# Optimization experiments

Measured on AMD Instinct MI355X. Metric: run time of the kernel, lower is better.

Reference implementation:

```python
import jax, jax.numpy as jnp
import numpy as np

B, DM, NH, NL, NP = 4, 768, 12, 3, 4
HD = DM // NH
H_IMG, W_IMG = 896, 896
LEVELS = [(H_IMG // 8, W_IMG // 8), (H_IMG // 16, W_IMG // 16), (H_IMG // 32, W_IMG // 32)]
QH, QW = H_IMG // 14, W_IMG // 14
LQ = QH * QW            # 4096 query tokens (stride-14 ViT grid)
LIN = sum(h * w for h, w in LEVELS)  # 16464 multi-scale value tokens


def setup_inputs() -> dict:
    key = jax.random.key(0)
    ks = jax.random.split(key, 14)
    s = 0.02
    return {
        "query": jax.random.normal(ks[0], (B, LQ, DM), jnp.float32),
        "feat": jax.random.normal(ks[1], (B, LIN, DM), jnp.float32),
        "ln_q_g": jnp.ones((DM,), jnp.float32),
        "ln_q_b": jnp.zeros((DM,), jnp.float32),
        "ln_f_g": jnp.ones((DM,), jnp.float32),
        "ln_f_b": jnp.zeros((DM,), jnp.float32),
        "W_off": jax.random.normal(ks[2], (DM, NH * NL * NP * 2), jnp.float32) * s,
        "b_off": jax.random.normal(ks[3], (NH * NL * NP * 2,), jnp.float32) * s,
        "W_attn": jax.random.normal(ks[4], (DM, NH * NL * NP), jnp.float32) * s,
        "b_attn": jax.random.normal(ks[5], (NH * NL * NP,), jnp.float32) * s,
        "W_val": jax.random.normal(ks[6], (DM, DM), jnp.float32) * s,
        "b_val": jnp.zeros((DM,), jnp.float32),
        "W_out": jax.random.normal(ks[7], (DM, DM), jnp.float32) * s,
        "b_out": jnp.zeros((DM,), jnp.float32),
        "gamma": jax.random.normal(ks[8], (DM,), jnp.float32) * s,
    }


def _ln(x, g, b, eps=1e-6):
    m = x.mean(-1, keepdims=True)
    v = ((x - m) ** 2).mean(-1, keepdims=True)
    return (x - m) * jax.lax.rsqrt(v + eps) * g + b


def _ref_points():
    # get_reference_points for the stride-14 query grid; pixel-center coords normalized
    ry, rx = jnp.meshgrid(
        (jnp.arange(QH, dtype=jnp.float32) + 0.5) / QH,
        (jnp.arange(QW, dtype=jnp.float32) + 0.5) / QW,
        indexing="ij",
    )
    return jnp.stack([rx.reshape(-1), ry.reshape(-1)], -1)  # (LQ, 2) in (x, y)


def _sample_level(v, loc, h_, w_):
    # v: (B, h_, w_, NH, HD); loc: (B, LQ, NH, NP, 2) normalized [0,1]
    # torch grid_sample bilinear, align_corners=False, zero padding
    x = loc[..., 0] * w_ - 0.5
    y = loc[..., 1] * h_ - 0.5
    x0 = jnp.floor(x)
    y0 = jnp.floor(y)
    wx = (x - x0)[..., None]
    wy = (y - y0)[..., None]
    x0i = x0.astype(jnp.int32)
    y0i = y0.astype(jnp.int32)
    bi = jnp.arange(B)[:, None, None, None]
    hi = jnp.arange(NH)[None, None, :, None]

    def g(yi, xi):
        valid = ((xi >= 0) & (xi < w_) & (yi >= 0) & (yi < h_)).astype(v.dtype)
        got = v[bi, jnp.clip(yi, 0, h_ - 1), jnp.clip(xi, 0, w_ - 1), hi]  # (B,LQ,NH,NP,HD)
        return got * valid[..., None]

    v00 = g(y0i, x0i)
    v01 = g(y0i, x0i + 1)
    v10 = g(y0i + 1, x0i)
    v11 = g(y0i + 1, x0i + 1)
    return v00 * (1 - wx) * (1 - wy) + v01 * wx * (1 - wy) + v10 * (1 - wx) * wy + v11 * wx * wy


def _injector(query, feat, ln_q_g, ln_q_b, ln_f_g, ln_f_b, W_off, b_off, W_attn, b_attn,
              W_val, b_val, W_out, b_out, gamma):
    q = _ln(query, ln_q_g, ln_q_b)
    f = _ln(feat, ln_f_g, ln_f_b)
    value = (f @ W_val + b_val).reshape(B, LIN, NH, HD)
    off = (q @ W_off + b_off).reshape(B, LQ, NH, NL, NP, 2)
    aw = jax.nn.softmax((q @ W_attn + b_attn).reshape(B, LQ, NH, NL * NP), axis=-1)
    aw = aw.reshape(B, LQ, NH, NL, NP)
    ref = _ref_points()  # (LQ, 2)
    offset_norm = jnp.array([[w, h] for h, w in LEVELS], jnp.float32)  # (NL, 2) = (W_, H_)
    loc = ref[None, :, None, None, None, :] + off / offset_norm[None, None, None, :, None, :]
    outs = []
    start = 0
    for lvl, (h_, w_) in enumerate(LEVELS):
        v = value[:, start:start + h_ * w_].reshape(B, h_, w_, NH, HD)
        outs.append(_sample_level(v, loc[:, :, :, lvl], h_, w_))
        start += h_ * w_
    samp = jnp.stack(outs, axis=3)  # (B, LQ, NH, NL, NP, HD)
    attn_out = (samp * aw[..., None]).sum(axis=(3, 4)).reshape(B, LQ, DM)
    attn_out = attn_out @ W_out + b_out
    return query + gamma * attn_out


def reference(query, feat, ln_q_g, ln_q_b, ln_f_g, ln_f_b, W_off, b_off, W_attn, b_attn,
              W_val, b_val, W_out, b_out, gamma):
    return _injector(query, feat, ln_q_g, ln_q_b, ln_f_g, ln_f_b, W_off, b_off, W_attn,
                     b_attn, W_val, b_val, W_out, b_out, gamma)
```

## Files before the change

kernel.cpp:

```cpp
#include <hip/hip_runtime.h>
#include <hip/hip_bf16.h>

typedef __hip_bfloat16 bf16;

#define BB    4
#define LQ    4096
#define LIN   16464
#define DM    768
#define NH    12
#define HD    64
#define K_DIM 768

typedef __attribute__((ext_vector_type(8))) __bf16 bfrag;
typedef __attribute__((ext_vector_type(4))) float  ffrag;

__device__ __forceinline__ void g2l16(const void* g, void* l) {
    __builtin_amdgcn_global_load_lds(
        (const __attribute__((address_space(1))) void*)g,
        (__attribute__((address_space(3))) void*)l, 16, 0, 0);
}

__device__ __forceinline__ int xcd_swz(int orig, int nwg) {
    int xcd = orig & 7, within = orig >> 3;
    int q = nwg >> 3, r = nwg & 7;
    return (xcd < r ? xcd * (q + 1) : r * (q + 1) + (xcd - r) * q) + within;
}

__global__ __launch_bounds__(256) void ln_kernel(
    const float* __restrict__ x, const float* __restrict__ g,
    const float* __restrict__ beta, bf16* __restrict__ y)
{
    int r = blockIdx.x * 4 + (threadIdx.x >> 6);
    int lane = threadIdx.x & 63;
    const float4* xr = (const float4*)(x + (size_t)r * DM);
    float4 v[3];
    #pragma unroll
    for (int i = 0; i < 3; i++) v[i] = xr[lane + 64 * i];
    float s = 0.f, ss = 0.f;
    #pragma unroll
    for (int i = 0; i < 3; i++) {
        s  += v[i].x + v[i].y + v[i].z + v[i].w;
        ss += v[i].x * v[i].x + v[i].y * v[i].y + v[i].z * v[i].z + v[i].w * v[i].w;
    }
    #pragma unroll
    for (int m = 1; m <= 32; m <<= 1) {
        s  += __shfl_xor(s, m);
        ss += __shfl_xor(ss, m);
    }
    float mean = s * (1.f / DM);
    float inv  = rsqrtf(ss * (1.f / DM) - mean * mean + 1e-6f);
    bf16* yr = y + (size_t)r * DM;
    #pragma unroll
    for (int i = 0; i < 3; i++) {
        float4 gg = ((const float4*)g)[lane + 64 * i];
        float4 bb = ((const float4*)beta)[lane + 64 * i];
        union { bf16 h[4]; uint2 u; } p;
        p.h[0] = __float2bfloat16((v[i].x - mean) * inv * gg.x + bb.x);
        p.h[1] = __float2bfloat16((v[i].y - mean) * inv * gg.y + bb.y);
        p.h[2] = __float2bfloat16((v[i].z - mean) * inv * gg.z + bb.z);
        p.h[3] = __float2bfloat16((v[i].w - mean) * inv * gg.w + bb.w);
        *(uint2*)(yr + (lane + 64 * i) * 4) = p.u;
    }
}

__global__ __launch_bounds__(256) void cast_transpose(
    const float* __restrict__ W, bf16* __restrict__ Wt, int N)
{
    __shared__ float t[32][33];
    int n0 = blockIdx.x * 32, k0 = blockIdx.y * 32;
    int tx = threadIdx.x & 31, ty = threadIdx.x >> 5;
    #pragma unroll
    for (int i = 0; i < 4; i++) {
        int k = k0 + ty + i * 8;
        int n = n0 + tx;
        t[ty + i * 8][tx] = (n < N) ? W[(size_t)k * N + n] : 0.f;
    }
    __syncthreads();
    #pragma unroll
    for (int i = 0; i < 4; i++) {
        int n = n0 + ty + i * 8;
        Wt[(size_t)n * K_DIM + k0 + tx] = __float2bfloat16(t[tx][ty + i * 8]);
    }
}

__global__ __launch_bounds__(256) void mfma_gemm(
    const bf16*  __restrict__ A,
    const bf16*  __restrict__ Bt,
    const float* __restrict__ bias,
    void*        __restrict__ C,
    const float* __restrict__ resid,
    const float* __restrict__ gamma,
    const float* __restrict__ bias2,
    int M, int N, int mode, int nsplit)
{
    __shared__ __align__(16) char lds[32768];

    int tid  = threadIdx.x;
    int lane = tid & 63;

    int nwg  = gridDim.x * gridDim.y;
    int orig = blockIdx.y * gridDim.x + blockIdx.x;
    int wg = xcd_swz(orig, nwg);
    int bn = (wg % gridDim.x) * 128;
    int bm = (wg / gridDim.x) * 128;

    int wave = tid >> 6;
    int wr = (wave & 1) * 64, wc = (wave >> 1) * 64;

    ffrag acc[4][4] = {};

    int c0 = tid, c1 = tid + 256;
    int r0 = c0 >> 2, kb0 = (c0 & 3) * 8;
    int r1 = c1 >> 2, kb1 = (c1 & 3) * 8;
    int ra0 = min(bm + r0, M - 1), ra1 = min(bm + r1, M - 1);
    const bf16* gA0 = A  + (size_t)ra0 * K_DIM + kb0;
    const bf16* gA1 = A  + (size_t)ra1 * K_DIM + kb1;
    const bf16* gB0 = Bt + (size_t)(bn + r0) * K_DIM + kb0;
    const bf16* gB1 = Bt + (size_t)(bn + r1) * K_DIM + kb1;

    int mrow = lane & 15;
    int kq   = (lane >> 4) * 8;

    for (int k0 = 0; k0 < K_DIM; k0 += 64) {
        #pragma unroll
        for (int s = 0; s < 2; s++) {
            char* As = lds + s * 16384;
            char* Bs = As + 8192;
            int ko = k0 + s * 32;
            g2l16(gA0 + ko, As + c0 * 16);
            g2l16(gA1 + ko, As + c1 * 16);
            g2l16(gB0 + ko, Bs + c0 * 16);
            g2l16(gB1 + ko, Bs + c1 * 16);
        }
        __syncthreads();
        #pragma unroll
        for (int s = 0; s < 2; s++) {
            char* As = lds + s * 16384;
            char* Bs = As + 8192;
            bfrag a[4], b[4];
            #pragma unroll
            for (int t = 0; t < 4; t++) {
                a[t] = *(const bfrag*)(As + ((wr + t * 16 + mrow) * 32 + kq) * 2);
                b[t] = *(const bfrag*)(Bs + ((wc + t * 16 + mrow) * 32 + kq) * 2);
            }
            #pragma unroll
            for (int i = 0; i < 4; i++)
                #pragma unroll
                for (int j = 0; j < 4; j++)
                    acc[i][j] = __builtin_amdgcn_mfma_f32_16x16x32_bf16(
                        a[i], b[j], acc[i][j], 0, 0, 0);
        }
        __syncthreads();
    }

    int q4 = (lane >> 4) * 4;
    #pragma unroll
    for (int i = 0; i < 4; i++) {
        #pragma unroll
        for (int rr = 0; rr < 4; rr++) {
            int rg = bm + wr + i * 16 + q4 + rr;
            if (rg < M) {
                #pragma unroll
                for (int j = 0; j < 4; j++) {
                    int cg = bn + wc + j * 16 + mrow;
                    if (cg < N) {
                        float bv = (mode == 3 && cg >= nsplit) ? bias2[cg - nsplit]
                                                               : bias[cg];
                        float v = acc[i][j][rr] + bv;
                        size_t idx = (size_t)rg * N + cg;
                        if (mode == 0)      ((bf16*)C)[idx]  = __float2bfloat16(v);
                        else if (mode == 2) ((float*)C)[idx] = resid[idx] + gamma[cg] * v;
                        else                ((float*)C)[idx] = v;
                    }
                }
            }
        }
    }
}

__global__ __launch_bounds__(256) void sample_kernel(
    const bf16*  __restrict__ value,
    const float* __restrict__ comb,
    bf16*        __restrict__ attn)
{
    int wg = xcd_swz(blockIdx.x, gridDim.x);
    int unit = __builtin_amdgcn_readfirstlane((wg << 2) + (threadIdx.x >> 6));
    int lane = threadIdx.x & 63;
    int o   = lane & 7;
    int c8  = lane >> 3;
    int k   = c8 & 3;
    int dx  = k & 1, dy = k >> 1;
    int h  = unit % NH;
    int bq = unit / NH;
    int q  = bq & (LQ - 1);
    int b  = bq >> 12;

    const float* rowp = comb + (size_t)bq * 432;
    const float* ob = rowp + h * 24;
    const float* lg = rowp + 288 + h * 12;

    float l[12];
    float mx = -1e30f;
    #pragma unroll
    for (int i = 0; i < 12; i++) { l[i] = lg[i]; mx = fmaxf(mx, l[i]); }
    float den = 0.f;
    #pragma unroll
    for (int i = 0; i < 12; i++) { l[i] = __expf(l[i] - mx); den += l[i]; }
    float rden = 1.f / den;
    #pragma unroll
    for (int i = 0; i < 12; i++) l[i] *= rden;

    float rx = ((q & 63) + 0.5f) * (1.f / 64.f);
    float ry = ((q >> 6) + 0.5f) * (1.f / 64.f);

    float acc[8] = {0.f};

    #pragma unroll
    for (int it = 0; it < 6; it++) {
        const int wl = (it < 2) ? 112 : (it < 4 ? 56 : 28);
        const int sl = (it < 2) ? 0   : (it < 4 ? 12544 : 15680);
        int s = it * 2 + ((lane >> 5) & 1);
        float ox = ob[s * 2 + 0];
        float oy = ob[s * 2 + 1];
        float x = rx * wl + ox - 0.5f;
        float y = ry * wl + oy - 0.5f;
        float xf = floorf(x), yf = floorf(y);
        float wx = x - xf,  wy = y - yf;
        int xi = (int)xf + dx;
        int yi = (int)yf + dy;
        bool valid = ((unsigned)xi < (unsigned)wl) & ((unsigned)yi < (unsigned)wl);
        int xc = min(max(xi, 0), wl - 1);
        int yc = min(max(yi, 0), wl - 1);
        int cell = b * LIN + sl + yc * wl + xc;
        const uint4* vp = (const uint4*)(value + ((size_t)cell * NH + h) * HD + o * 8);
        uint4 v = *vp;
        float aw = (lane & 32) ? l[it * 2 + 1] : l[it * 2];
        float bw = (dx ? wx : 1.f - wx) * (dy ? wy : 1.f - wy);
        float w = valid ? aw * bw : 0.f;
        const unsigned* u = (const unsigned*)&v;
        #pragma unroll
        for (int j = 0; j < 4; j++) {
            float f0 = __uint_as_float(u[j] << 16);
            float f1 = __uint_as_float(u[j] & 0xFFFF0000u);
            acc[j * 2 + 0] = fmaf(w, f0, acc[j * 2 + 0]);
            acc[j * 2 + 1] = fmaf(w, f1, acc[j * 2 + 1]);
        }
    }

    #pragma unroll
    for (int m = 8; m <= 32; m <<= 1) {
        #pragma unroll
        for (int j = 0; j < 8; j++)
            acc[j] += __shfl_xor(acc[j], m);
    }

    if (c8 == 0) {
        union { bf16 h8[8]; uint4 u4; } r;
        #pragma unroll
        for (int j = 0; j < 8; j++) r.h8[j] = __float2bfloat16(acc[j]);
        *(uint4*)(attn + (size_t)bq * DM + h * HD + o * 8) = r.u4;
    }
}

extern "C" void kernel_launch(void* const* d_in, const int* in_sizes, int n_in,
                              void* d_out, int out_size, void* d_ws, size_t ws_size,
                              hipStream_t stream)
{
    const float* query  = (const float*)d_in[0];
    const float* feat   = (const float*)d_in[1];
    const float* ln_q_g = (const float*)d_in[2];
    const float* ln_q_b = (const float*)d_in[3];
    const float* ln_f_g = (const float*)d_in[4];
    const float* ln_f_b = (const float*)d_in[5];
    const float* W_off  = (const float*)d_in[6];
    const float* b_off  = (const float*)d_in[7];
    const float* W_attn = (const float*)d_in[8];
    const float* b_attn = (const float*)d_in[9];
    const float* W_val  = (const float*)d_in[10];
    const float* b_val  = (const float*)d_in[11];
    const float* W_out  = (const float*)d_in[12];
    const float* b_out  = (const float*)d_in[13];
    const float* gamma  = (const float*)d_in[14];
    float* out = (float*)d_out;

    char* ws = (char*)d_ws;
    char* od = (char*)d_out;
    const int M_F = BB * LIN;
    const int M_Q = BB * LQ;

    bf16*  value  = (bf16*)(ws);
    bf16*  f_ln   = (bf16*)(ws + 101154816);
    bf16*  Wt_out = (bf16*)(ws + 101154816);
    bf16*  q_ln   = (bf16*)(ws + 202309632);
    bf16*  attn   = (bf16*)(ws + 202309632);

    bf16*  Wt_val  = (bf16*)(od);
    bf16*  Wt_comb = (bf16*)(od + 1179648);
    float* comb    = (float*)(od + 2162688);

    cast_transpose<<<dim3(24, 24), 256, 0, stream>>>(W_val, Wt_val, 768);
    cast_transpose<<<dim3(9, 24), 256, 0, stream>>>(W_off, Wt_comb, 288);
    cast_transpose<<<dim3(7, 24), 256, 0, stream>>>(
        W_attn, Wt_comb + (size_t)288 * K_DIM, 144);

    ln_kernel<<<M_F / 4, 256, 0, stream>>>(feat, ln_f_g, ln_f_b, f_ln);
    ln_kernel<<<M_Q / 4, 256, 0, stream>>>(query, ln_q_g, ln_q_b, q_ln);

    mfma_gemm<<<dim3(6, (M_F + 127) / 128), 256, 0, stream>>>(
        f_ln, Wt_val, b_val, value, nullptr, nullptr, nullptr, M_F, DM, 0, 0);

    cast_transpose<<<dim3(24, 24), 256, 0, stream>>>(W_out, Wt_out, 768);

    mfma_gemm<<<dim3(4, M_Q / 128), 256, 0, stream>>>(
        q_ln, Wt_comb, b_off, comb, nullptr, nullptr, b_attn, M_Q, 432, 3, 288);

    sample_kernel<<<(M_Q * NH) / 4, 256, 0, stream>>>(value, comb, attn);

    mfma_gemm<<<dim3(6, M_Q / 128), 256, 0, stream>>>(
        attn, Wt_out, b_out, out, query, gamma, nullptr, M_Q, DM, 2, 0);
}
```

Baseline: 797.5 us.

## Triple-buffer GEMM LDS staging with vmcnt waits and XOR-swizzled layout

Replaces the load-all-then-compute loop of the MFMA GEMM with a three-stage ring of 32-wide K tiles in LDS. Prefetches are issued three tiles ahead and gated by s_waitcnt vmcnt, so global loads overlap the MFMA work instead of stalling at a full __syncthreads. It also XOR-swizzles the K chunk offset per row on both store and load to reduce LDS bank conflicts. LDS use grows from 32KB to 48KB per block, which may lower occupancy, and the hand-counted vmcnt values depend on the exact load count per stage.

```diff
diff --git a/kernel.cpp b/kernel.cpp
--- a/kernel.cpp
+++ b/kernel.cpp
@@ -93,7 +93,7 @@
     const float* __restrict__ bias2,
     int M, int N, int mode, int nsplit)
 {
-    __shared__ __align__(16) char lds[32768];
+    __shared__ __align__(16) char lds[49152];
 
     int tid  = threadIdx.x;
     int lane = tid & 63;
@@ -109,48 +109,56 @@
 
     ffrag acc[4][4] = {};
 
-    int c0 = tid, c1 = tid + 256;
-    int r0 = c0 >> 2, kb0 = (c0 & 3) * 8;
-    int r1 = c1 >> 2, kb1 = (c1 & 3) * 8;
-    int ra0 = min(bm + r0, M - 1), ra1 = min(bm + r1, M - 1);
-    const bf16* gA0 = A  + (size_t)ra0 * K_DIM + kb0;
-    const bf16* gA1 = A  + (size_t)ra1 * K_DIM + kb1;
-    const bf16* gB0 = Bt + (size_t)(bn + r0) * K_DIM + kb0;
-    const bf16* gB1 = Bt + (size_t)(bn + r1) * K_DIM + kb1;
+    int rA = tid >> 2;
+    int kb = (((tid & 3) ^ ((rA >> 1) & 3)) * 8);
+    int ra0 = min(bm + rA, M - 1), ra1 = min(bm + 64 + rA, M - 1);
+    const bf16* gA0 = A  + (size_t)ra0 * K_DIM + kb;
+    const bf16* gA1 = A  + (size_t)ra1 * K_DIM + kb;
+    const bf16* gB0 = Bt + (size_t)(bn + rA) * K_DIM + kb;
+    const bf16* gB1 = Bt + (size_t)(bn + 64 + rA) * K_DIM + kb;
 
     int mrow = lane & 15;
-    int kq   = (lane >> 4) * 8;
-
-    for (int k0 = 0; k0 < K_DIM; k0 += 64) {
-        #pragma unroll
-        for (int s = 0; s < 2; s++) {
-            char* As = lds + s * 16384;
-            char* Bs = As + 8192;
-            int ko = k0 + s * 32;
-            g2l16(gA0 + ko, As + c0 * 16);
-            g2l16(gA1 + ko, As + c1 * 16);
-            g2l16(gB0 + ko, Bs + c0 * 16);
-            g2l16(gB1 + ko, Bs + c1 * 16);
+    int kqs  = (((lane >> 4) ^ ((mrow >> 1) & 3)) * 8);
+
+    auto stage = [&](char* buf, int kt) {
+        const int ko = kt * 32;
+        g2l16(gA0 + ko, buf + tid * 16);
+        g2l16(gA1 + ko, buf + tid * 16 + 4096);
+        g2l16(gB0 + ko, buf + 8192 + tid * 16);
+        g2l16(gB1 + ko, buf + 8192 + tid * 16 + 4096);
+    };
+
+    char* b0 = lds;
+    char* b1 = lds + 16384;
+    char* b2 = lds + 32768;
+    stage(b0, 0); stage(b1, 1); stage(b2, 2);
+
+    #pragma unroll
+    for (int kt = 0; kt < 24; kt++) {
+        if (kt + 2 < 24)      asm volatile("s_waitcnt vmcnt(8)" ::: "memory");
+        else if (kt + 1 < 24) asm volatile("s_waitcnt vmcnt(4)" ::: "memory");
+        else                  asm volatile("s_waitcnt vmcnt(0)" ::: "memory");
+        __builtin_amdgcn_s_barrier();
+        __builtin_amdgcn_sched_barrier(0);
+
+        bfrag a[4], b[4];
+        #pragma unroll
+        for (int t = 0; t < 4; t++) {
+            a[t] = *(const bfrag*)(b0 + ((wr + t * 16 + mrow) * 32 + kqs) * 2);
+            b[t] = *(const bfrag*)(b0 + 8192 + ((wc + t * 16 + mrow) * 32 + kqs) * 2);
         }
-        __syncthreads();
-        #pragma unroll
-        for (int s = 0; s < 2; s++) {
-            char* As = lds + s * 16384;
-            char* Bs = As + 8192;
-            bfrag a[4], b[4];
+        #pragma unroll
+        for (int i = 0; i < 4; i++)
             #pragma unroll
-            for (int t = 0; t < 4; t++) {
-                a[t] = *(const bfrag*)(As + ((wr + t * 16 + mrow) * 32 + kq) * 2);
-                b[t] = *(const bfrag*)(Bs + ((wc + t * 16 + mrow) * 32 + kq) * 2);
-            }
-            #pragma unroll
-            for (int i = 0; i < 4; i++)
-                #pragma unroll
-                for (int j = 0; j < 4; j++)
-                    acc[i][j] = __builtin_amdgcn_mfma_f32_16x16x32_bf16(
-                        a[i], b[j], acc[i][j], 0, 0, 0);
-        }
-        __syncthreads();
+            for (int j = 0; j < 4; j++)
+                acc[i][j] = __builtin_amdgcn_mfma_f32_16x16x32_bf16(
+                    a[i], b[j], acc[i][j], 0, 0, 0);
+
+        __builtin_amdgcn_sched_barrier(0);
+        __builtin_amdgcn_s_barrier();
+        __builtin_amdgcn_sched_barrier(0);
+        if (kt + 3 < 24) stage(b0, kt + 3);
+        char* tp = b0; b0 = b1; b1 = b2; b2 = tp;
     }
 
     int q4 = (lane >> 4) * 4;
```

Measured after the change: 776.5 us. -2.6%, faster.
